# Kernel tuning notes

Hardware: AMD Instinct MI355X
Metric: run time of the kernel (lower is better)

Reference implementation:

```python
import jax, jax.numpy as jnp
import numpy as np

SOS_TOKEN = 0
EOS_TOKEN = 29
B, S, ENC = 128, 400, 512   # batch, encoder max seq len, encoder feature dim
E, H, D, P, V = 256, 512, 128, 128, 30  # embed, dec hidden, dec out, attn proj, vocab
T = 600  # inference timesteps


def setup_inputs() -> dict:
    key = jax.random.key(0)
    ks = jax.random.split(key, 20)
    u = lambda k, sh: jax.random.uniform(k, sh, jnp.float32, -0.1, 0.1)
    n = lambda k, sh, s=0.02: s * jax.random.normal(k, sh, jnp.float32)
    embed = n(ks[0], (V, E), 1.0).at[EOS_TOKEN].set(0.0)  # padding_idx=EOS
    inp = dict(
        encoder_outputs=jax.random.normal(ks[1], (B, S, ENC), jnp.float32),
        encoder_lens=jax.random.randint(ks[2], (B,), S // 2, S + 1),
        embed=embed,
        W_ih1=u(ks[3], (4 * H, E + P)), W_hh1=u(ks[4], (4 * H, H)),
        b_ih1=u(ks[5], (4 * H,)), b_hh1=u(ks[6], (4 * H,)),
        W_ih2=u(ks[7], (4 * D, H)), W_hh2=u(ks[8], (4 * D, D)),
        b_ih2=u(ks[9], (4 * D,)), b_hh2=u(ks[10], (4 * D,)),
        Wk=n(ks[11], (P, ENC)), bk=jnp.zeros((P,), jnp.float32),
        Wv=n(ks[12], (P, ENC)), bv=jnp.zeros((P,), jnp.float32),
        Wq=n(ks[13], (P, D)), bq=jnp.zeros((P,), jnp.float32),
        b_char=jnp.zeros((V,), jnp.float32),
    )
    return inp


def _lstm_cell(x, h, c, W_ih, W_hh, b_ih, b_hh):
    gates = x @ W_ih.T + h @ W_hh.T + b_ih + b_hh
    i, f, g, o = jnp.split(gates, 4, axis=-1)
    c2 = jax.nn.sigmoid(f) * c + jax.nn.sigmoid(i) * jnp.tanh(g)
    return jax.nn.sigmoid(o) * jnp.tanh(c2), c2


def reference(encoder_outputs, encoder_lens, embed,
              W_ih1, W_hh1, b_ih1, b_hh1,
              W_ih2, W_hh2, b_ih2, b_hh2,
              Wk, bk, Wv, bv, Wq, bq, b_char):
    # precompute attention keys/values and mask (set_key_value_mask)
    keyv = encoder_outputs @ Wk.T + bk           # [B, S, P]
    valv = encoder_outputs @ Wv.T + bv           # [B, S, P]
    mask = jnp.arange(S)[None, :] < encoder_lens[:, None]  # [B, S]
    scale = 1.0 / np.sqrt(P).astype(np.float32)

    char0 = jnp.full((B,), SOS_TOKEN, jnp.int32)
    h1 = jnp.zeros((B, H), jnp.float32); c1 = jnp.zeros((B, H), jnp.float32)
    h2 = jnp.zeros((B, D), jnp.float32); c2 = jnp.zeros((B, D), jnp.float32)
    ctx0 = jnp.zeros((B, P), jnp.float32)

    def step(carry, _):
        char, h1, c1, h2, c2, ctx = carry
        ce = embed[char]                                   # [B, E]
        x = jnp.concatenate([ce, ctx], axis=1)
        h1n, c1n = _lstm_cell(x, h1, c1, W_ih1, W_hh1, b_ih1, b_hh1)
        h2n, c2n = _lstm_cell(h1n, h2, c2, W_ih2, W_hh2, b_ih2, b_hh2)
        q = h2n @ Wq.T + bq                                # [B, P] (attention.query)
        e = jnp.einsum('bsp,bp->bs', keyv, q) * scale
        w = jax.nn.softmax(jnp.where(mask, e, -1e9), axis=-1)
        ctxn = jnp.einsum('bs,bsp->bp', w, valv)           # [B, P]
        out_emb = jnp.concatenate([q, ctxn], axis=1)       # [B, P+P] == [B, E]
        pred = out_emb @ embed.T + b_char                  # tied char_prob weight
        charn = jnp.argmax(pred, axis=1).astype(jnp.int32)
        return (charn, h1n, c1n, h2n, c2n, ctxn), (pred, w[0])

    _, (preds, attn0) = jax.lax.scan(step, (char0, h1, c1, h2, c2, ctx0), None, length=T)
    predictions = jnp.transpose(preds, (1, 0, 2))  # [B, T, V]
    attention_plot = attn0                          # [T, S]
    return predictions, attention_plot
```

## Files before the change

### kernel.cpp

```cpp
#include <hip/hip_runtime.h>
#include <math.h>

#define B_   128
#define S_   400
#define ENC_ 512
#define E_   256
#define H_   512
#define D_   128
#define P_   128
#define V_   30
#define T_   600

#define KEYV_OFF 0
#define VALV_OFF (KEYV_OFF + B_*S_*P_)
#define H1_OFF   (VALV_OFF + B_*S_*P_)
#define H2T_OFF  (H1_OFF + 2*H_*B_)
#define H2R_OFF  (H2T_OFF + 2*D_*B_)
#define CTXT_OFF (H2R_OFF + B_*D_)
#define CHR_OFF  (CTXT_OFF + P_*B_)
#define PV0_OFF  (CHR_OFF + B_)
#define MS0_OFF  (PV0_OFF + B_*P_)
#define ES0_OFF  (MS0_OFF + 2*B_)
#define FLAG_OFF (ES0_OFF + 200)
#define WS_FLOATS (FLAG_OFF + B_*32)

#define PRED_N (B_*T_*V_)
#define NBLK 256
#define NTHR 512

#define W1_BASE 0
#define W2_BASE 14336
#define SCR     24576
#define LDS_FLOATS (SCR + 13120)

__device__ __forceinline__ float sigm_(float x){ return 1.0f/(1.0f + expf(-x)); }

__device__ __forceinline__ float ldA(const float* p){
  return __hip_atomic_load(p, __ATOMIC_RELAXED, __HIP_MEMORY_SCOPE_AGENT);
}
__device__ __forceinline__ void stA(float* p, float v){
  __hip_atomic_store(p, v, __ATOMIC_RELAXED, __HIP_MEMORY_SCOPE_AGENT);
}
__device__ __forceinline__ int ldAi(const int* p){
  return __hip_atomic_load(p, __ATOMIC_RELAXED, __HIP_MEMORY_SCOPE_AGENT);
}
__device__ __forceinline__ void stAi(int* p, int v){
  __hip_atomic_store(p, v, __ATOMIC_RELAXED, __HIP_MEMORY_SCOPE_AGENT);
}
__device__ __forceinline__ void ldA2f(const float* p, float& a, float& b){
  unsigned long long v = __hip_atomic_load((const unsigned long long*)p,
                         __ATOMIC_RELAXED, __HIP_MEMORY_SCOPE_AGENT);
  a = __uint_as_float((unsigned)v);
  b = __uint_as_float((unsigned)(v>>32));
}

__device__ __forceinline__ void gbar(int* bar){
  asm volatile("s_waitcnt vmcnt(0)" ::: "memory");
  __syncthreads();
  if (threadIdx.x == 0){
    const int g0 = __hip_atomic_load(bar, __ATOMIC_RELAXED, __HIP_MEMORY_SCOPE_AGENT);
    asm volatile("" ::: "memory");
    int* leaf = bar + 64 + (blockIdx.x & 7)*32;
    int lo = __hip_atomic_fetch_add(leaf, 1, __ATOMIC_RELAXED, __HIP_MEMORY_SCOPE_AGENT);
    bool done = false;
    if (lo == 31){
      int ro = __hip_atomic_fetch_add(bar+32, 1, __ATOMIC_RELAXED, __HIP_MEMORY_SCOPE_AGENT);
      if (ro == 7){
        #pragma unroll
        for (int i=0;i<8;++i)
          __hip_atomic_store(bar+64+i*32, 0, __ATOMIC_RELAXED, __HIP_MEMORY_SCOPE_AGENT);
        __hip_atomic_store(bar+32, 0, __ATOMIC_RELAXED, __HIP_MEMORY_SCOPE_AGENT);
        asm volatile("s_waitcnt vmcnt(0)" ::: "memory");
        __hip_atomic_fetch_add(bar, 1, __ATOMIC_RELAXED, __HIP_MEMORY_SCOPE_AGENT);
        done = true;
      }
    }
    if (!done){
      while (__hip_atomic_load(bar, __ATOMIC_RELAXED, __HIP_MEMORY_SCOPE_AGENT) == g0)
        __builtin_amdgcn_s_sleep(4);
    }
  }
  __syncthreads();
}

__global__ __launch_bounds__(256) void k_kv(const float* __restrict__ enc,
    const float* __restrict__ Wk, const float* __restrict__ bk,
    const float* __restrict__ Wv, const float* __restrict__ bv,
    float* __restrict__ ws)
{
  __shared__ float As[32][68];
  __shared__ float Bs[32][68];
  const int tid = threadIdx.x;
  const int tx = tid & 15, ty = tid >> 4;
  const int n0 = blockIdx.x * 64;
  const int c0 = blockIdx.y * 64;
  float acc[4][4] = {};
  for (int k0 = 0; k0 < ENC_; k0 += 32){
    #pragma unroll
    for (int i = 0; i < 8; ++i){
      int idx = tid + 256*i;
      int kk = idx & 31, nl = idx >> 5;
      As[kk][nl] = enc[(size_t)(n0+nl)*ENC_ + k0 + kk];
    }
    #pragma unroll
    for (int i = 0; i < 8; ++i){
      int idx = tid + 256*i;
      int kk = idx & 31, cl = idx >> 5;
      int c = c0 + cl; int p = c & 127;
      const float* W = (c < 128) ? Wk : Wv;
      Bs[kk][cl] = W[(size_t)p*ENC_ + k0 + kk];
    }
    __syncthreads();
    #pragma unroll
    for (int kk = 0; kk < 32; ++kk){
      float4 a4 = *(const float4*)&As[kk][ty*4];
      float4 b4 = *(const float4*)&Bs[kk][tx*4];
      float aa[4] = {a4.x, a4.y, a4.z, a4.w};
      float bb[4] = {b4.x, b4.y, b4.z, b4.w};
      #pragma unroll
      for (int i=0;i<4;++i)
        #pragma unroll
        for (int j=0;j<4;++j) acc[i][j] += aa[i]*bb[j];
    }
    __syncthreads();
  }
  float* keyv = ws + KEYV_OFF;
  float* valv = ws + VALV_OFF;
  #pragma unroll
  for (int i=0;i<4;++i){
    int n = n0 + ty*4 + i; int b = n / S_; int s = n - b*S_;
    #pragma unroll
    for (int j=0;j<4;++j){
      int c = c0 + tx*4 + j;
      float v = acc[i][j];
      if (c < 128) keyv[((size_t)b*S_+s)*P_ + c]       = v + bk[c];
      else         valv[((size_t)b*S_+s)*P_ + (c-128)] = v + bv[c-128];
    }
  }
}

__global__ __launch_bounds__(NTHR, 1) void k_persist(
    const float* __restrict__ embed,
    const float* __restrict__ Wih1, const float* __restrict__ Whh1,
    const float* __restrict__ bih1, const float* __restrict__ bhh1,
    const float* __restrict__ Wih2, const float* __restrict__ Whh2,
    const float* __restrict__ bih2, const float* __restrict__ bhh2,
    const float* __restrict__ Wq, const float* __restrict__ bq,
    const float* __restrict__ bchar, const int* __restrict__ lens,
    float* ws, float* out)
{
  extern __shared__ float smem[];
  const int tid = threadIdx.x;
  const int bid = blockIdx.x;
  int* bar = (int*)(ws + WS_FLOATS);

  float* ctxT = ws + CTXT_OFF;
  int*   chrg = (int*)(ws + CHR_OFF);
  float* h2R  = ws + H2R_OFF;
  float* pv0g = ws + PV0_OFF;
  float* ms0g = ws + MS0_OFF;
  float* es0g = ws + ES0_OFF;
  int*   flag = (int*)(ws + FLAG_OFF);

  float* Wl  = smem + W1_BASE;
  float* W2l = smem + W2_BASE;
  float* scr = smem + SCR;

  const int lane = tid & 63;
  const int so8  = tid >> 6;

  const int ib = bid & 1, ug = bid >> 1, b0 = ib*64;
  const int iq = lane & 15, rq = lane >> 4;
  const int u1 = tid >> 6;
  const int J1 = ug*4 + (u1 & 3);
  const int sA  = (tid & 31)*2;
  const int kbA = tid >> 5;

  const int ig2 = bid & 3, ug2 = bid >> 2, b02 = ig2*32;
  const int iq2 = lane & 7, rq2 = lane >> 3;
  const int u2 = tid >> 5;
  const int J2 = ug2*4 + (u2 & 3);
  const int sB  = (tid & 15)*2;
  const int kbB = tid >> 4;

  const int h3  = bid >> 7;
  const int it3 = bid & 127;
  const float* keyv3 = ws + KEYV_OFF + (size_t)it3*S_*P_;
  const float* valv3 = ws + VALV_OFF + (size_t)it3*S_*P_;
  const int lenb = lens[it3];
  const int cw  = h3 ? (lenb - 200) : 200;
  const int s0w = h3*200;
  const float bqr  = bq[tid >> 2];
  const float bchr = ((tid >> 4) < V_) ? bchar[tid >> 4] : 0.f;

  {
    const int r = tid & 15, kb = tid >> 4;
    const int R = (r >> 2)*H_ + ug*4 + (r & 3);
    for (int j = 0; j < 28; ++j){
      int k = kb*28 + j;
      float v = (k < 384) ? Wih1[(size_t)R*384 + k] : Whh1[(size_t)R*H_ + (k-384)];
      Wl[k*16 + r] = v;
    }
  }
  if (bid < 128){
    const int r = tid & 15, kb = tid >> 4;
    const int R = (r >> 2)*D_ + ug2*4 + (r & 3);
    for (int j = 0; j < 20; ++j){
      int k = kb*20 + j;
      float v = (k < 512) ? Wih2[(size_t)R*H_ + k] : Whh2[(size_t)R*D_ + (k-512)];
      W2l[k*16 + r] = v;
    }
  }
  __syncthreads();

  float c1r = 0.f, c2r = 0.f;
  float b1s[4], b2s[4];
  #pragma unroll
  for (int g=0; g<4; ++g){
    b1s[g] = bih1[g*H_ + J1] + bhh1[g*H_ + J1];
    b2s[g] = (bid < 128) ? (bih2[g*D_ + J2] + bhh2[g*D_ + J2]) : 0.f;
  }

  for (int t = 0; t < T_; ++t){
    {
      const float* h1oT = ws + H1_OFF + (size_t)(t&1)*H_*B_;
      float*       h1nT = ws + H1_OFF + (size_t)((t+1)&1)*H_*B_;
      float* Xs  = scr;
      float* red = scr + 4096;
      int*   schs= (int*)(scr + 12800);

      if (tid < 64) schs[tid] = ldAi(chrg + b0 + tid);
      __syncthreads();
      const int chA = schs[sA], chB = schs[sA+1];

      float xr[4][8];
      auto LOADX = [&](int p, float* dst){
        if (p < 4){
          const float4 va = *(const float4*)(embed + (size_t)chA*E_ + p*64 + kbA*4);
          const float4 vb = *(const float4*)(embed + (size_t)chB*E_ + p*64 + kbA*4);
          dst[0]=va.x; dst[1]=vb.x; dst[2]=va.y; dst[3]=vb.y;
          dst[4]=va.z; dst[5]=vb.z; dst[6]=va.w; dst[7]=vb.w;
        } else {
          const float* base = (p < 6) ? (ctxT + (size_t)(p*64-256)*B_)
                                      : (h1oT + (size_t)(p*64-384)*B_);
          #pragma unroll
          for (int j=0;j<4;++j)
            ldA2f(base + (size_t)(kbA*4+j)*B_ + b0 + sA, dst[j*2], dst[j*2+1]);
        }
      };
      LOADX(0,xr[0]); LOADX(1,xr[1]); LOADX(2,xr[2]); LOADX(3,xr[3]);

      float acc[4][4] = {};
      #pragma unroll
      for (int p = 0; p < 14; ++p){
        float* xc = xr[p&3];
        #pragma unroll
        for (int j=0;j<4;++j){
          const int kl = kbA*4 + j;
          *(float2*)&Xs[kl*64 + (((sA>>2)+kl)&15)*4 + (sA&3)]
            = make_float2(xc[j*2], xc[j*2+1]);
        }
        __syncthreads();
        if (p + 4 < 14) LOADX(p + 4, xr[p&3]);
        float4 xv[8], wv[8];
        #pragma unroll
        for (int it = 0; it < 8; ++it){
          const int kl = so8*8 + it;
          xv[it] = *(const float4*)&Xs[kl*64 + ((iq + kl)&15)*4];
          wv[it] = *(const float4*)&Wl[(p*64 + kl)*16 + rq*4];
        }
        #pragma unroll
        for (int it = 0; it < 8; ++it){
          float xa[4] = {xv[it].x, xv[it].y, xv[it].z, xv[it].w};
          float wa[4] = {wv[it].x, wv[it].y, wv[it].z, wv[it].w};
          #pragma unroll
          for (int i=0;i<4;++i)
            #pragma unroll
            for (int j=0;j<4;++j) acc[i][j] += xa[i]*wa[j];
        }
        __syncthreads();
      }
      #pragma unroll
      for (int j=0;j<4;++j)
        *(float4*)&red[so8*1088 + (rq*4+j)*68 + iq*4]
          = make_float4(acc[0][j], acc[1][j], acc[2][j], acc[3][j]);
      __syncthreads();
      if (tid < 256){
        const int item = tid & 63;
        float gate[4];
        #pragma unroll
        for (int g=0; g<4; ++g){
          float s = 0.f;
          #pragma unroll
          for (int w=0; w<8; ++w) s += red[w*1088 + (g*4+(u1&3))*68 + item];
          gate[g] = s + b1s[g];
        }
        float cn = sigm_(gate[1])*c1r + sigm_(gate[0])*tanhf(gate[2]);
        float hn = sigm_(gate[3])*tanhf(cn);
        c1r = cn;
        stA(h1nT + (size_t)J1*B_ + b0 + item, hn);
      }
    }
    gbar(bar);

    if (bid < 128){
      const float* h1nT = ws + H1_OFF + (size_t)((t+1)&1)*H_*B_;
      const float* h2oT = ws + H2T_OFF + (size_t)(t&1)*D_*B_;
      float*       h2nT = ws + H2T_OFF + (size_t)((t+1)&1)*D_*B_;
      float* Xs2  = scr;
      float* red2 = scr + 2048;

      float xr2[4][4];
      auto LOADX2 = [&](int p, float* dst){
        const float* base = (p < 8) ? (h1nT + (size_t)(p*64)*B_)
                                    : (h2oT + (size_t)(p*64-512)*B_);
        #pragma unroll
        for (int j=0;j<2;++j)
          ldA2f(base + (size_t)(kbB*2+j)*B_ + b02 + sB, dst[j*2], dst[j*2+1]);
      };
      LOADX2(0,xr2[0]); LOADX2(1,xr2[1]); LOADX2(2,xr2[2]); LOADX2(3,xr2[3]);

      float acc2[4][2] = {};
      #pragma unroll
      for (int p = 0; p < 10; ++p){
        float* xc = xr2[p&3];
        #pragma unroll
        for (int j=0;j<2;++j){
          const int kl = kbB*2 + j;
          *(float2*)&Xs2[kl*32 + (((sB>>2)+kl)&7)*4 + (sB&3)]
            = make_float2(xc[j*2], xc[j*2+1]);
        }
        __syncthreads();
        if (p + 4 < 10) LOADX2(p + 4, xr2[p&3]);
        float4 xv2[8]; float2 wv2[8];
        #pragma unroll
        for (int it = 0; it < 8; ++it){
          const int kl = so8*8 + it;
          xv2[it] = *(const float4*)&Xs2[kl*32 + ((iq2 + kl)&7)*4];
          wv2[it] = *(const float2*)&W2l[(p*64 + kl)*16 + rq2*2];
        }
        #pragma unroll
        for (int it = 0; it < 8; ++it){
          float xa[4] = {xv2[it].x, xv2[it].y, xv2[it].z, xv2[it].w};
          #pragma unroll
          for (int i=0;i<4;++i){
            acc2[i][0] += xa[i]*wv2[it].x;
            acc2[i][1] += xa[i]*wv2[it].y;
          }
        }
        __syncthreads();
      }
      #pragma unroll
      for (int j=0;j<2;++j)
        *(float4*)&red2[so8*576 + (rq2*2+j)*36 + iq2*4]
          = make_float4(acc2[0][j], acc2[1][j], acc2[2][j], acc2[3][j]);
      __syncthreads();
      if (tid < 128){
        const int item = tid & 31;
        float gate[4];
        #pragma unroll
        for (int g=0; g<4; ++g){
          float s = 0.f;
          #pragma unroll
          for (int w=0; w<8; ++w) s += red2[w*576 + (g*4+(u2&3))*36 + item];
          gate[g] = s + b2s[g];
        }
        float cn = sigm_(gate[1])*c2r + sigm_(gate[0])*tanhf(gate[2]);
        float hn = sigm_(gate[3])*tanhf(cn);
        c2r = cn;
        stA(h2nT + (size_t)J2*B_ + b02 + item, hn);
        stA(h2R  + (size_t)(b02+item)*D_ + J2, hn);
      }
    }
    gbar(bar);

    {
      float* es3  = scr;
      float* hs3  = scr + 208;
      float* qs3  = scr + 336;
      float* redw = scr + 464;
      float* red33= scr + 480;
      float* pvc  = scr + 2592;
      float* oes3 = scr + 2720;
      float* pred3= scr + 2976;

      if (tid < 208) es3[tid] = 0.f;
      if (tid < 128) hs3[tid] = ldA(h2R + (size_t)it3*D_ + tid);
      __syncthreads();
      {
        const int r = tid >> 2, kq = tid & 3;
        const float* wr = Wq + (size_t)r*D_ + kq*32;
        float a = 0.f;
        #pragma unroll
        for (int j=0;j<8;++j){
          float4 wvq = *(const float4*)(wr + j*4);
          float4 hv = *(const float4*)&hs3[kq*32 + j*4];
          a += wvq.x*hv.x + wvq.y*hv.y + wvq.z*hv.z + wvq.w*hv.w;
        }
        a += __shfl_down(a, 2, 4);
        a += __shfl_down(a, 1, 4);
        if (kq == 0) qs3[r] = a + bqr;
      }
      __syncthreads();
      const int r2 = tid >> 1, hseg = tid & 1;
      float sv = -INFINITY;
      if (r2 < cw){
        const float4* kr = (const float4*)(keyv3 + (size_t)(s0w + r2)*P_ + hseg*64);
        float a = 0.f;
        #pragma unroll 8
        for (int d=0; d<16; ++d){
          float4 kv = kr[d];
          float4 qv = *(const float4*)&qs3[hseg*64 + d*4];
          a += kv.x*qv.x + kv.y*qv.y + kv.z*qv.z + kv.w*qv.w;
        }
        a += __shfl_down(a, 1, 2);
        if (hseg == 0) sv = a * 0.08838834764831845f;
      }
      float mv = sv;
      #pragma unroll
      for (int o=32; o; o>>=1) mv = fmaxf(mv, __shfl_xor(mv, o));
      if ((tid & 63) == 0) redw[tid >> 6] = mv;
      __syncthreads();
      const float mh = fmaxf(fmaxf(fmaxf(redw[0],redw[1]),fmaxf(redw[2],redw[3])),
                             fmaxf(fmaxf(redw[4],redw[5]),fmaxf(redw[6],redw[7])));
      float pvx = 0.f;
      if (r2 < cw && hseg == 0){ pvx = expf(sv - mh); es3[r2] = pvx; }
      float sm = pvx;
      #pragma unroll
      for (int o=32; o; o>>=1) sm += __shfl_xor(sm, o);
      if ((tid & 63) == 0) redw[8 + (tid >> 6)] = sm;
      __syncthreads();
      const float sumh = ((redw[8]+redw[9])+(redw[10]+redw[11]))
                       + ((redw[12]+redw[13])+(redw[14]+redw[15]));
      {
        const int p4 = tid & 31, sg = tid >> 5;
        float a0=0,a1=0,a2=0,a3=0;
        const int rbeg = sg*13, rend = min(rbeg + 13, cw);
        for (int r = rbeg; r < rend; ++r){
          float e = es3[r];
          float4 v = *(const float4*)(valv3 + (size_t)(s0w + r)*P_ + p4*4);
          a0 += e*v.x; a1 += e*v.y; a2 += e*v.z; a3 += e*v.w;
        }
        *(float4*)&red33[sg*132 + p4*4] = make_float4(a0,a1,a2,a3);
      }
      __syncthreads();

      if (h3 == 0){
        if (tid < 128){
          float c = 0.f;
          #pragma unroll
          for (int sg=0; sg<16; ++sg) c += red33[sg*132 + tid];
          stA(pv0g + (size_t)it3*P_ + tid, c);
        }
        if (tid == 0){ stA(ms0g + it3*2, mh); stA(ms0g + it3*2 + 1, sumh); }
        if (it3 == 0 && tid < 200) stA(es0g + tid, es3[tid]);
        asm volatile("s_waitcnt vmcnt(0)" ::: "memory");
        __syncthreads();
        if (tid == 0) stAi(flag + it3*32, t + 1);
      } else {
        if (tid < 128){
          float c = 0.f;
          #pragma unroll
          for (int sg=0; sg<16; ++sg) c += red33[sg*132 + tid];
          pvc[tid] = c;
        }
        __syncthreads();
        if (tid == 0){
          while (ldAi(flag + it3*32) != t + 1) __builtin_amdgcn_s_sleep(1);
        }
        __syncthreads();
        asm volatile("" ::: "memory");
        const float m0 = ldA(ms0g + it3*2), s0v = ldA(ms0g + it3*2 + 1);
        const float m  = fmaxf(m0, mh);
        const float e0 = expf(m0 - m), e1 = expf(mh - m);
        const float sum = s0v*e0 + sumh*e1;
        if (tid < 128){
          float c = (ldA(pv0g + (size_t)it3*P_ + tid)*e0 + pvc[tid]*e1) / sum;
          stA(ctxT + (size_t)tid*B_ + it3, c);
          oes3[tid] = qs3[tid]; oes3[128+tid] = c;
        }
        __syncthreads();
        {
          const int v = tid >> 4, k16 = tid & 15;
          float a = 0.f;
          if (v < V_){
            const float4* er = (const float4*)(embed + (size_t)v*E_ + k16*16);
            #pragma unroll
            for (int j=0;j<4;++j){
              float4 ev = er[j];
              float4 ov = *(const float4*)&oes3[k16*16 + j*4];
              a += ev.x*ov.x + ev.y*ov.y + ev.z*ov.z + ev.w*ov.w;
            }
          }
          a += __shfl_down(a, 8, 16);
          a += __shfl_down(a, 4, 16);
          a += __shfl_down(a, 2, 16);
          a += __shfl_down(a, 1, 16);
          if (v < V_ && k16 == 0){
            float pvv = a + bchr;
            pred3[v] = pvv;
            out[((size_t)it3*T_ + t)*V_ + v] = pvv;
          }
        }
        __syncthreads();
        if (tid < 32){
          float val = (tid < V_) ? pred3[tid] : -INFINITY;
          int idx = tid;
          #pragma unroll
          for (int o = 16; o > 0; o >>= 1){
            float ov = __shfl_down(val, o, 32);
            int oi = __shfl_down(idx, o, 32);
            if (ov > val || (ov == val && oi < idx)){ val = ov; idx = oi; }
          }
          if (tid == 0) stAi(chrg + it3, idx);
        }
        if (it3 == 0 && tid < S_){
          float v = (tid < 200) ? ldA(es0g + tid)*e0 : es3[tid - 200]*e1;
          out[PRED_N + (size_t)t*S_ + tid] = v / sum;
        }
      }
    }
    gbar(bar);
  }
}

extern "C" void kernel_launch(void* const* d_in, const int* in_sizes, int n_in,
                              void* d_out, int out_size, void* d_ws, size_t ws_size,
                              hipStream_t stream)
{
  (void)in_sizes; (void)n_in; (void)out_size; (void)ws_size;
  const float* enc   = (const float*)d_in[0];
  const int*   lens  = (const int*)d_in[1];
  const float* embed = (const float*)d_in[2];
  const float* Wih1  = (const float*)d_in[3];
  const float* Whh1  = (const float*)d_in[4];
  const float* bih1  = (const float*)d_in[5];
  const float* bhh1  = (const float*)d_in[6];
  const float* Wih2  = (const float*)d_in[7];
  const float* Whh2  = (const float*)d_in[8];
  const float* bih2  = (const float*)d_in[9];
  const float* bhh2  = (const float*)d_in[10];
  const float* Wk    = (const float*)d_in[11];
  const float* bk    = (const float*)d_in[12];
  const float* Wv    = (const float*)d_in[13];
  const float* bv    = (const float*)d_in[14];
  const float* Wq    = (const float*)d_in[15];
  const float* bq    = (const float*)d_in[16];
  const float* bchar = (const float*)d_in[17];
  float* out = (float*)d_out;
  float* ws  = (float*)d_ws;

  hipMemsetAsync((char*)d_ws + (size_t)H1_OFF*sizeof(float), 0,
                 (size_t)(WS_FLOATS - H1_OFF)*sizeof(float) + 2048, stream);
  hipLaunchKernelGGL(k_kv, dim3(800,4), dim3(256), 0, stream, enc, Wk, bk, Wv, bv, ws);

  hipFuncSetAttribute((const void*)k_persist,
                      hipFuncAttributeMaxDynamicSharedMemorySize, LDS_FLOATS*4);
  hipLaunchKernelGGL(k_persist, dim3(NBLK), dim3(NTHR), LDS_FLOATS*4, stream,
                     embed, Wih1, Whh1, bih1, bhh1,
                     Wih2, Whh2, bih2, bhh2,
                     Wq, bq, bchar, lens, ws, out);
}
```

Before: 22.31 ms.

## Fold Wq into precomputed keys to remove query projection from critical path

Adds a pre-pass kernel that multiplies the projected keys by Wq (and computes a key·bq bias term), so attention scores can be computed directly from h2 without first computing q. The q projection moves after the cross-block flag wait, where it is only needed for the output embedding, shortening the serial per-step chain. It also rebalances the two attention halves (split at 144 instead of 200, to match encoder lengths of 200 to 400) and widens the grid barrier tree to 16 leaves of 16 blocks. The extra pre-pass adds a one-time cost and changes the floating-point summation order.

```diff
diff --git a/kernel.cpp b/kernel.cpp
--- a/kernel.cpp
+++ b/kernel.cpp
@@ -10,6 +10,8 @@
 #define P_   128
 #define V_   30
 #define T_   600
+
+#define RSPLIT 144
 
 #define KEYV_OFF 0
 #define VALV_OFF (KEYV_OFF + B_*S_*P_)
@@ -22,7 +24,8 @@
 #define MS0_OFF  (PV0_OFF + B_*P_)
 #define ES0_OFF  (MS0_OFF + 2*B_)
 #define FLAG_OFF (ES0_OFF + 200)
-#define WS_FLOATS (FLAG_OFF + B_*32)
+#define KB0_OFF  (FLAG_OFF + B_*32)
+#define WS_FLOATS (KB0_OFF + B_*S_)
 
 #define PRED_N (B_*T_*V_)
 #define NBLK 256
@@ -60,14 +63,14 @@
   if (threadIdx.x == 0){
     const int g0 = __hip_atomic_load(bar, __ATOMIC_RELAXED, __HIP_MEMORY_SCOPE_AGENT);
     asm volatile("" ::: "memory");
-    int* leaf = bar + 64 + (blockIdx.x & 7)*32;
+    int* leaf = bar + 64 + (blockIdx.x & 15)*32;
     int lo = __hip_atomic_fetch_add(leaf, 1, __ATOMIC_RELAXED, __HIP_MEMORY_SCOPE_AGENT);
     bool done = false;
-    if (lo == 31){
+    if (lo == 15){
       int ro = __hip_atomic_fetch_add(bar+32, 1, __ATOMIC_RELAXED, __HIP_MEMORY_SCOPE_AGENT);
-      if (ro == 7){
-        #pragma unroll
-        for (int i=0;i<8;++i)
+      if (ro == 15){
+        #pragma unroll
+        for (int i=0;i<16;++i)
           __hip_atomic_store(bar+64+i*32, 0, __ATOMIC_RELAXED, __HIP_MEMORY_SCOPE_AGENT);
         __hip_atomic_store(bar+32, 0, __ATOMIC_RELAXED, __HIP_MEMORY_SCOPE_AGENT);
         asm volatile("s_waitcnt vmcnt(0)" ::: "memory");
@@ -139,6 +142,62 @@
   }
 }
 
+__global__ __launch_bounds__(256) void k_k2(const float* __restrict__ Wq,
+    const float* __restrict__ bq, float* __restrict__ ws)
+{
+  __shared__ float As[32][68];
+  __shared__ float Bs[32][132];
+  __shared__ float bqs[32];
+  float* keyv = ws + KEYV_OFF;
+  float* kb0  = ws + KB0_OFF;
+  const int tid = threadIdx.x;
+  const int n0 = blockIdx.x * 64;
+  const int ty = tid >> 4;
+  const int tx = tid & 15;
+  float acc[4][8] = {};
+  float kbacc[4] = {};
+  for (int k0 = 0; k0 < 128; k0 += 32){
+    #pragma unroll
+    for (int i = 0; i < 8; ++i){
+      int idx = tid + 256*i;
+      int kk = idx & 31, nl = idx >> 5;
+      As[kk][nl] = keyv[(size_t)(n0+nl)*P_ + k0 + kk];
+    }
+    #pragma unroll
+    for (int i = 0; i < 16; ++i){
+      int idx = tid + 256*i;
+      int kk = idx >> 7, d = idx & 127;
+      Bs[kk][d] = Wq[(size_t)(k0+kk)*D_ + d];
+    }
+    if (tid < 32) bqs[tid] = bq[k0 + tid];
+    __syncthreads();
+    #pragma unroll
+    for (int kk = 0; kk < 32; ++kk){
+      float4 a4 = *(const float4*)&As[kk][ty*4];
+      float aa[4] = {a4.x, a4.y, a4.z, a4.w};
+      const float* br = &Bs[kk][tx*8];
+      #pragma unroll
+      for (int i=0;i<4;++i){
+        #pragma unroll
+        for (int j=0;j<8;++j) acc[i][j] += aa[i]*br[j];
+      }
+      if (tx == 0){
+        float bv = bqs[kk];
+        #pragma unroll
+        for (int i=0;i<4;++i) kbacc[i] += bv*aa[i];
+      }
+    }
+    __syncthreads();
+  }
+  #pragma unroll
+  for (int i=0;i<4;++i){
+    int row = n0 + ty*4 + i;
+    *(float4*)&keyv[(size_t)row*P_ + tx*8]     = make_float4(acc[i][0],acc[i][1],acc[i][2],acc[i][3]);
+    *(float4*)&keyv[(size_t)row*P_ + tx*8 + 4] = make_float4(acc[i][4],acc[i][5],acc[i][6],acc[i][7]);
+    if (tx == 0) kb0[row] = kbacc[i];
+  }
+}
+
 __global__ __launch_bounds__(NTHR, 1) void k_persist(
     const float* __restrict__ embed,
     const float* __restrict__ Wih1, const float* __restrict__ Whh1,
@@ -161,6 +220,7 @@
   float* ms0g = ws + MS0_OFF;
   float* es0g = ws + ES0_OFF;
   int*   flag = (int*)(ws + FLAG_OFF);
+  float* kb0g = ws + KB0_OFF;
 
   float* Wl  = smem + W1_BASE;
   float* W2l = smem + W2_BASE;
@@ -185,11 +245,12 @@
 
   const int h3  = bid >> 7;
   const int it3 = bid & 127;
-  const float* keyv3 = ws + KEYV_OFF + (size_t)it3*S_*P_;
+  const float* k2_3  = ws + KEYV_OFF + (size_t)it3*S_*P_;
   const float* valv3 = ws + VALV_OFF + (size_t)it3*S_*P_;
+  const float* kb0_3 = kb0g + (size_t)it3*S_;
   const int lenb = lens[it3];
-  const int cw  = h3 ? (lenb - 200) : 200;
-  const int s0w = h3*200;
+  const int cw  = h3 ? (lenb - RSPLIT) : RSPLIT;
+  const int s0w = h3*RSPLIT;
   const float bqr  = bq[tid >> 2];
   const float bchr = ((tid >> 4) < V_) ? bchar[tid >> 4] : 0.f;
 
@@ -376,45 +437,31 @@
 
     {
       float* es3  = scr;
-      float* hs3  = scr + 208;
-      float* qs3  = scr + 336;
-      float* redw = scr + 464;
-      float* red33= scr + 480;
-      float* pvc  = scr + 2592;
-      float* oes3 = scr + 2720;
-      float* pred3= scr + 2976;
-
-      if (tid < 208) es3[tid] = 0.f;
+      float* hs3  = scr + 260;
+      float* qs3  = scr + 388;
+      float* redw = scr + 516;
+      float* red33= scr + 532;
+      float* pvc  = scr + 2644;
+      float* oes3 = scr + 2772;
+      float* pred3= scr + 3028;
+
+      if (tid < 260) es3[tid] = 0.f;
       if (tid < 128) hs3[tid] = ldA(h2R + (size_t)it3*D_ + tid);
-      __syncthreads();
-      {
-        const int r = tid >> 2, kq = tid & 3;
-        const float* wr = Wq + (size_t)r*D_ + kq*32;
-        float a = 0.f;
-        #pragma unroll
-        for (int j=0;j<8;++j){
-          float4 wvq = *(const float4*)(wr + j*4);
-          float4 hv = *(const float4*)&hs3[kq*32 + j*4];
-          a += wvq.x*hv.x + wvq.y*hv.y + wvq.z*hv.z + wvq.w*hv.w;
-        }
-        a += __shfl_down(a, 2, 4);
-        a += __shfl_down(a, 1, 4);
-        if (kq == 0) qs3[r] = a + bqr;
-      }
       __syncthreads();
       const int r2 = tid >> 1, hseg = tid & 1;
       float sv = -INFINITY;
       if (r2 < cw){
-        const float4* kr = (const float4*)(keyv3 + (size_t)(s0w + r2)*P_ + hseg*64);
+        const float4* kr = (const float4*)(k2_3 + (size_t)(s0w + r2)*P_ + hseg*64);
+        float kb0v = kb0_3[s0w + r2];
         float a = 0.f;
         #pragma unroll 8
         for (int d=0; d<16; ++d){
           float4 kv = kr[d];
-          float4 qv = *(const float4*)&qs3[hseg*64 + d*4];
-          a += kv.x*qv.x + kv.y*qv.y + kv.z*qv.z + kv.w*qv.w;
+          float4 hv = *(const float4*)&hs3[hseg*64 + d*4];
+          a += kv.x*hv.x + kv.y*hv.y + kv.z*hv.z + kv.w*hv.w;
         }
         a += __shfl_down(a, 1, 2);
-        if (hseg == 0) sv = a * 0.08838834764831845f;
+        if (hseg == 0) sv = (a + kb0v) * 0.08838834764831845f;
       }
       float mv = sv;
       #pragma unroll
@@ -434,8 +481,9 @@
                        + ((redw[12]+redw[13])+(redw[14]+redw[15]));
       {
         const int p4 = tid & 31, sg = tid >> 5;
+        const int chunk = (cw + 15) >> 4;
+        const int rbeg = sg*chunk, rend = min(rbeg + chunk, cw);
         float a0=0,a1=0,a2=0,a3=0;
-        const int rbeg = sg*13, rend = min(rbeg + 13, cw);
         for (int r = rbeg; r < rend; ++r){
           float e = es3[r];
           float4 v = *(const float4*)(valv3 + (size_t)(s0w + r)*P_ + p4*4);
@@ -453,7 +501,7 @@
           stA(pv0g + (size_t)it3*P_ + tid, c);
         }
         if (tid == 0){ stA(ms0g + it3*2, mh); stA(ms0g + it3*2 + 1, sumh); }
-        if (it3 == 0 && tid < 200) stA(es0g + tid, es3[tid]);
+        if (it3 == 0 && tid < RSPLIT) stA(es0g + tid, es3[tid]);
         asm volatile("s_waitcnt vmcnt(0)" ::: "memory");
         __syncthreads();
         if (tid == 0) stAi(flag + it3*32, t + 1);
@@ -470,6 +518,21 @@
         }
         __syncthreads();
         asm volatile("" ::: "memory");
+        {
+          const int r = tid >> 2, kq = tid & 3;
+          const float* wr = Wq + (size_t)r*D_ + kq*32;
+          float a = 0.f;
+          #pragma unroll
+          for (int j=0;j<8;++j){
+            float4 wvq = *(const float4*)(wr + j*4);
+            float4 hv = *(const float4*)&hs3[kq*32 + j*4];
+            a += wvq.x*hv.x + wvq.y*hv.y + wvq.z*hv.z + wvq.w*hv.w;
+          }
+          a += __shfl_down(a, 2, 4);
+          a += __shfl_down(a, 1, 4);
+          if (kq == 0) qs3[r] = a + bqr;
+        }
+        __syncthreads();
         const float m0 = ldA(ms0g + it3*2), s0v = ldA(ms0g + it3*2 + 1);
         const float m  = fmaxf(m0, mh);
         const float e0 = expf(m0 - m), e1 = expf(mh - m);
@@ -515,7 +578,7 @@
           if (tid == 0) stAi(chrg + it3, idx);
         }
         if (it3 == 0 && tid < S_){
-          float v = (tid < 200) ? ldA(es0g + tid)*e0 : es3[tid - 200]*e1;
+          float v = (tid < RSPLIT) ? ldA(es0g + tid)*e0 : es3[tid - RSPLIT]*e1;
           out[PRED_N + (size_t)t*S_ + tid] = v / sum;
         }
       }
@@ -551,8 +614,9 @@
   float* ws  = (float*)d_ws;
 
   hipMemsetAsync((char*)d_ws + (size_t)H1_OFF*sizeof(float), 0,
-                 (size_t)(WS_FLOATS - H1_OFF)*sizeof(float) + 2048, stream);
+                 (size_t)(WS_FLOATS - H1_OFF)*sizeof(float) + 4096, stream);
   hipLaunchKernelGGL(k_kv, dim3(800,4), dim3(256), 0, stream, enc, Wk, bk, Wv, bv, ws);
+  hipLaunchKernelGGL(k_k2, dim3(800),   dim3(256), 0, stream, Wq, bq, ws);
 
   hipFuncSetAttribute((const void*)k_persist,
                       hipFuncAttributeMaxDynamicSharedMemorySize, LDS_FLOATS*4);
```

After: 23.90 ms. +7.1%, slower.
